# Optimization experiments

Hardware: AMD Instinct MI355X
Metric: run time of the kernel (lower is better)

The kernel has to match this reference:

```python
import jax, jax.numpy as jnp
import numpy as np

NPOINTS = 4096


def farthest_point_sample(inp, npoints):
    """Iterative farthest point sampling.
    inp: [B, N, 3] float. Returns (out [B, npoints, 3], idx [B, npoints] int32).
    Matches the CUDA kernel semantics: first selected index is 0, running
    min-squared-distance buffer initialized to a large value (temp=1e10),
    each step picks the point farthest from the selected set.
    """
    B, N, _ = inp.shape
    init_idx = jnp.zeros((B,), dtype=jnp.int32)
    dist0 = jnp.full((B, N), 1e10, dtype=inp.dtype)

    def step(carry, _):
        dist, last_idx = carry
        # gather last selected point per batch: [B, 1, 3]
        last_pt = jnp.take_along_axis(inp, last_idx[:, None, None].astype(jnp.int32), axis=1)
        d = jnp.sum((inp - last_pt) ** 2, axis=-1)  # [B, N]
        dist = jnp.minimum(dist, d)
        nxt = jnp.argmax(dist, axis=-1).astype(jnp.int32)  # [B]
        return (dist, nxt), nxt

    (_, _), rest = jax.lax.scan(step, (dist0, init_idx), None, length=npoints - 1)
    idx = jnp.concatenate([init_idx[None, :], rest], axis=0).T  # [B, npoints]
    out = jnp.take_along_axis(inp, idx[..., None], axis=1)  # [B, npoints, 3]
    return out, idx


def setup_inputs() -> dict:
    key = jax.random.key(0)
    inp = jax.random.normal(key, (32, 131072, 3), dtype=jnp.float32)
    return {"inp": inp}


def reference(inp):
    return farthest_point_sample(inp, NPOINTS)
```

## Files before the change

kernel.cpp:

```cpp
#include <hip/hip_runtime.h>
#include <stdint.h>

#define NBATCH  32
#define NPTS    131072
#define NPOINTS 4096
#define BPB     8
#define TPB     512
#define PPT     32
#define PPB     (NPTS / BPB)

typedef unsigned long long u64;
typedef unsigned int u32;


__global__ __attribute__((amdgpu_flat_work_group_size(TPB, TPB)))
           __attribute__((amdgpu_waves_per_eu(2, 2)))
void fps_kernel(const float* __restrict__ inp, float* __restrict__ out,
                u64* __restrict__ slots)
{
#pragma clang fp contract(off)
    const int bid  = blockIdx.x;
    const int b    = bid & 31;
    const int j    = bid >> 5;
    const int t    = threadIdx.x;
    const int lane = t & 63;
    const int wid  = t >> 6;

    const float* P  = inp + (size_t)b * NPTS * 3;
    float* outP     = out + (size_t)b * NPOINTS * 3;
    float* outIdx   = out + (size_t)NBATCH * NPOINTS * 3 + (size_t)b * NPOINTS;

    const int base = j * PPB;

    float px[PPT], py[PPT], pz[PPT], dist[PPT];
#pragma unroll
    for (int k = 0; k < PPT; ++k) {
        const int p = base + k * TPB + t;
        const float* pp = P + (size_t)p * 3;
        px[k] = pp[0]; py[k] = pp[1]; pz[k] = pp[2];
        asm volatile("" : "+v"(px[k]), "+v"(py[k]), "+v"(pz[k]));
        dist[k] = 1e10f;
    }

    float qx = P[0], qy = P[1], qz = P[2];

    if (j == 0 && t == 0) {
        outP[0] = qx; outP[1] = qy; outP[2] = qz;
        outIdx[0] = 0.0f;
    }

    u64* myslots = slots + (size_t)b * (2 * BPB * 2);

    __shared__ u64 skey[TPB / 64];
    __shared__ float sq[3];

    for (int it = 0; it < NPOINTS - 1; ++it) {
        float m = -1.0f; int ki = 0;
#pragma unroll
        for (int k = 0; k < PPT; ++k) {
            float dx = px[k] - qx;
            float dy = py[k] - qy;
            float dz = pz[k] - qz;
            float yy = dy * dy;
            asm("" : "+v"(yy));
            float d  = __builtin_fmaf(dz, dz,
                        __builtin_fmaf(dx, dx, yy));
            float nd = fminf(dist[k], d);
            dist[k] = nd;
            if (nd > m) { m = nd; ki = k; }
        }
        const int gi = base + ki * TPB + t;
        u64 key = ((u64)__float_as_uint(m) << 17) | (u64)(131071 - gi);

#pragma unroll
        for (int s = 1; s < 64; s <<= 1) {
            u64 o = __shfl_xor(key, s, 64);
            if (o > key) key = o;
        }
        if (lane == 0) skey[wid] = key;
        __syncthreads();

        if (wid == 0) {
            u64 k2 = (lane < TPB / 64) ? skey[lane] : 0ull;
#pragma unroll
            for (int s = 1; s < TPB / 64; s <<= 1) {
                u64 o = __shfl_xor(k2, s, 64);
                if (o > k2) k2 = o;
            }
            const int par = it & 1;
            const u64 tag = (u64)(it + 1) << 49;
            if (lane == 0) {
                __hip_atomic_store(&myslots[(par * BPB + j) * 2], tag | k2,
                                   __ATOMIC_RELEASE, __HIP_MEMORY_SCOPE_AGENT);
            }
            u64 v = 0;
            bool ok = (lane >= BPB);
            int guard = 0;
            while (true) {
                if (!ok) {
                    v = __hip_atomic_load(&myslots[(par * BPB + lane) * 2 + 0],
                                          __ATOMIC_ACQUIRE, __HIP_MEMORY_SCOPE_AGENT);
                    ok = (v >> 49) >= (u64)(it + 1);
                }
                if (__all((int)ok)) break;
                if (++guard > (1 << 20)) break;
            }
            u64 k3 = (lane < BPB) ? (v & ((1ull << 49) - 1)) : 0ull;
#pragma unroll
            for (int s = 1; s < BPB; s <<= 1) {
                u64 o = __shfl_xor(k3, s, 64);
                if (o > k3) k3 = o;
            }
            const int wgi = 131071 - (int)(k3 & 0x1FFFF);
            if (lane == 0) {
                const float* qp = P + (size_t)wgi * 3;
                float nqx = qp[0], nqy = qp[1], nqz = qp[2];
                sq[0] = nqx; sq[1] = nqy; sq[2] = nqz;
                if (j == 0) {
                    float* o3 = outP + (size_t)(it + 1) * 3;
                    o3[0] = nqx; o3[1] = nqy; o3[2] = nqz;
                    outIdx[it + 1] = (float)wgi;
                }
            }
        }
        __syncthreads();
        qx = sq[0]; qy = sq[1]; qz = sq[2];
    }
}

extern "C" void kernel_launch(void* const* d_in, const int* in_sizes, int n_in,
                              void* d_out, int out_size, void* d_ws, size_t ws_size,
                              hipStream_t stream)
{
    const float* inp = (const float*)d_in[0];
    float* outp      = (float*)d_out;
    u64* slots       = (u64*)d_ws;

    hipMemsetAsync(d_ws, 0, (size_t)NBATCH * 2 * BPB * 2 * sizeof(u64), stream);

    fps_kernel<<<NBATCH * BPB, TPB, 0, stream>>>(inp, outp, slots);
}
```

Measured before the change: 19.88 ms.

## Move point x,y coordinates from registers into LDS and pad sync slots

Per-thread x and y coordinates now live in shared memory as float2 and are read back each iteration, while z and the running distance stay in registers. The waves_per_eu hint is removed. Sync slots are spaced 8 u64 apart instead of 2, so each slot sits on its own 64-byte line. The aim is to cut VGPR pressure and reduce false sharing on the flags, at the cost of LDS reads in the hot loop and 128KB of LDS per block.

```diff
diff --git a/kernel.cpp b/kernel.cpp
--- a/kernel.cpp
+++ b/kernel.cpp
@@ -12,13 +12,16 @@
 typedef unsigned long long u64;
 typedef unsigned int u32;
 
+#define SLOT_STRIDE 8
+
 
 __global__ __attribute__((amdgpu_flat_work_group_size(TPB, TPB)))
-           __attribute__((amdgpu_waves_per_eu(2, 2)))
 void fps_kernel(const float* __restrict__ inp, float* __restrict__ out,
                 u64* __restrict__ slots)
 {
 #pragma clang fp contract(off)
+    extern __shared__ float2 XY[];
+
     const int bid  = blockIdx.x;
     const int b    = bid & 31;
     const int j    = bid >> 5;
@@ -32,13 +35,15 @@
 
     const int base = j * PPB;
 
-    float px[PPT], py[PPT], pz[PPT], dist[PPT];
+    float pz[PPT], dist[PPT];
 #pragma unroll
     for (int k = 0; k < PPT; ++k) {
-        const int p = base + k * TPB + t;
-        const float* pp = P + (size_t)p * 3;
-        px[k] = pp[0]; py[k] = pp[1]; pz[k] = pp[2];
-        asm volatile("" : "+v"(px[k]), "+v"(py[k]), "+v"(pz[k]));
+        const int l = k * TPB + t;
+        const float* pp = P + (size_t)(base + l) * 3;
+        float x = pp[0], y = pp[1], z = pp[2];
+        XY[l] = make_float2(x, y);
+        pz[k] = z;
+        asm volatile("" : "+v"(pz[k]));
         dist[k] = 1e10f;
     }
 
@@ -49,17 +54,20 @@
         outIdx[0] = 0.0f;
     }
 
-    u64* myslots = slots + (size_t)b * (2 * BPB * 2);
+    u64* myslots = slots + (size_t)b * (2 * BPB * SLOT_STRIDE);
 
     __shared__ u64 skey[TPB / 64];
     __shared__ float sq[3];
+
+    __syncthreads();
 
     for (int it = 0; it < NPOINTS - 1; ++it) {
         float m = -1.0f; int ki = 0;
 #pragma unroll
         for (int k = 0; k < PPT; ++k) {
-            float dx = px[k] - qx;
-            float dy = py[k] - qy;
+            float2 xy = XY[k * TPB + t];
+            float dx = xy.x - qx;
+            float dy = xy.y - qy;
             float dz = pz[k] - qz;
             float yy = dy * dy;
             asm("" : "+v"(yy));
@@ -90,7 +98,7 @@
             const int par = it & 1;
             const u64 tag = (u64)(it + 1) << 49;
             if (lane == 0) {
-                __hip_atomic_store(&myslots[(par * BPB + j) * 2], tag | k2,
+                __hip_atomic_store(&myslots[(par * BPB + j) * SLOT_STRIDE], tag | k2,
                                    __ATOMIC_RELEASE, __HIP_MEMORY_SCOPE_AGENT);
             }
             u64 v = 0;
@@ -98,7 +106,7 @@
             int guard = 0;
             while (true) {
                 if (!ok) {
-                    v = __hip_atomic_load(&myslots[(par * BPB + lane) * 2 + 0],
+                    v = __hip_atomic_load(&myslots[(par * BPB + lane) * SLOT_STRIDE],
                                           __ATOMIC_ACQUIRE, __HIP_MEMORY_SCOPE_AGENT);
                     ok = (v >> 49) >= (u64)(it + 1);
                 }
@@ -136,7 +144,8 @@
     float* outp      = (float*)d_out;
     u64* slots       = (u64*)d_ws;
 
-    hipMemsetAsync(d_ws, 0, (size_t)NBATCH * 2 * BPB * 2 * sizeof(u64), stream);
+    hipMemsetAsync(d_ws, 0,
+                   (size_t)NBATCH * 2 * BPB * SLOT_STRIDE * sizeof(u64), stream);
 
-    fps_kernel<<<NBATCH * BPB, TPB, 0, stream>>>(inp, outp, slots);
+    fps_kernel<<<NBATCH * BPB, TPB, (size_t)PPB * sizeof(float2), stream>>>(inp, outp, slots);
 }
```

Result: slower. 22.62 ms (+13.8%).

## Double blocks per batch and carry winner coordinates through reduction slots

Applied to the files above, without the earlier changes.

Splits each batch across 16 blocks instead of 8, with 16 points per thread, and raises waves per EU to 4. This spreads the per-iteration distance update over more CUs. Each thread now tracks the coordinates of its best point and passes them through the wave, block and cross-block reductions. The coordinates are published in padded global slots, so the dependent global gather of the winning point is no longer needed. The cost is more blocks taking part in the spin-wait barrier and extra slot stores and loads per iteration.

```diff
diff --git a/kernel.cpp b/kernel.cpp
--- a/kernel.cpp
+++ b/kernel.cpp
@@ -4,17 +4,19 @@
 #define NBATCH  32
 #define NPTS    131072
 #define NPOINTS 4096
-#define BPB     8
+#define BPB     16
 #define TPB     512
-#define PPT     32
+#define PPT     16
 #define PPB     (NPTS / BPB)
 
 typedef unsigned long long u64;
 typedef unsigned int u32;
 
+#define SLOT_STRIDE 8
+
 
 __global__ __attribute__((amdgpu_flat_work_group_size(TPB, TPB)))
-           __attribute__((amdgpu_waves_per_eu(2, 2)))
+           __attribute__((amdgpu_waves_per_eu(4, 4)))
 void fps_kernel(const float* __restrict__ inp, float* __restrict__ out,
                 u64* __restrict__ slots)
 {
@@ -38,24 +40,25 @@
         const int p = base + k * TPB + t;
         const float* pp = P + (size_t)p * 3;
         px[k] = pp[0]; py[k] = pp[1]; pz[k] = pp[2];
-        asm volatile("" : "+v"(px[k]), "+v"(py[k]), "+v"(pz[k]));
         dist[k] = 1e10f;
     }
 
     float qx = P[0], qy = P[1], qz = P[2];
-
     if (j == 0 && t == 0) {
         outP[0] = qx; outP[1] = qy; outP[2] = qz;
         outIdx[0] = 0.0f;
     }
 
-    u64* myslots = slots + (size_t)b * (2 * BPB * 2);
+    u64* myslots = slots + (size_t)b * (2 * BPB * SLOT_STRIDE);
 
     __shared__ u64 skey[TPB / 64];
+    __shared__ u64 sxy[TPB / 64];
+    __shared__ u64 sz[TPB / 64];
     __shared__ float sq[3];
 
     for (int it = 0; it < NPOINTS - 1; ++it) {
         float m = -1.0f; int ki = 0;
+        float mx = 0.f, my = 0.f, mz = 0.f;
 #pragma unroll
         for (int k = 0; k < PPT; ++k) {
             float dx = px[k] - qx;
@@ -67,59 +70,82 @@
                         __builtin_fmaf(dx, dx, yy));
             float nd = fminf(dist[k], d);
             dist[k] = nd;
-            if (nd > m) { m = nd; ki = k; }
+            bool c = nd > m;
+            m  = c ? nd : m;  ki = c ? k : ki;
+            mx = c ? px[k] : mx; my = c ? py[k] : my; mz = c ? pz[k] : mz;
         }
         const int gi = base + ki * TPB + t;
         u64 key = ((u64)__float_as_uint(m) << 17) | (u64)(131071 - gi);
 
+        u64 kmax = key;
 #pragma unroll
         for (int s = 1; s < 64; s <<= 1) {
-            u64 o = __shfl_xor(key, s, 64);
-            if (o > key) key = o;
+            u64 o = __shfl_xor(kmax, s, 64);
+            if (o > kmax) kmax = o;
         }
-        if (lane == 0) skey[wid] = key;
+        int wl = __ffsll(__ballot(key == kmax)) - 1;
+        float wx = __shfl(mx, wl, 64), wy = __shfl(my, wl, 64), wz = __shfl(mz, wl, 64);
+        if (lane == 0) {
+            skey[wid] = kmax;
+            sxy[wid]  = ((u64)__float_as_uint(wy) << 32) | __float_as_uint(wx);
+            sz[wid]   = __float_as_uint(wz);
+        }
         __syncthreads();
 
         if (wid == 0) {
             u64 k2 = (lane < TPB / 64) ? skey[lane] : 0ull;
+            u64 kk = k2;
 #pragma unroll
             for (int s = 1; s < TPB / 64; s <<= 1) {
-                u64 o = __shfl_xor(k2, s, 64);
-                if (o > k2) k2 = o;
+                u64 o = __shfl_xor(kk, s, 64);
+                if (o > kk) kk = o;
             }
+            int we = __ffsll(__ballot(k2 == kk && lane < TPB / 64)) - 1;
             const int par = it & 1;
             const u64 tag = (u64)(it + 1) << 49;
             if (lane == 0) {
-                __hip_atomic_store(&myslots[(par * BPB + j) * 2], tag | k2,
-                                   __ATOMIC_RELEASE, __HIP_MEMORY_SCOPE_AGENT);
+                u64* slot = &myslots[(size_t)(par * BPB + j) * SLOT_STRIDE];
+                __hip_atomic_store(&slot[1], sxy[we], __ATOMIC_RELAXED, __HIP_MEMORY_SCOPE_AGENT);
+                __hip_atomic_store(&slot[2], sz[we],  __ATOMIC_RELAXED, __HIP_MEMORY_SCOPE_AGENT);
+                __hip_atomic_store(&slot[0], tag | kk, __ATOMIC_RELEASE, __HIP_MEMORY_SCOPE_AGENT);
             }
-            u64 v = 0;
+            u64 tw = 0;
             bool ok = (lane >= BPB);
             int guard = 0;
             while (true) {
                 if (!ok) {
-                    v = __hip_atomic_load(&myslots[(par * BPB + lane) * 2 + 0],
-                                          __ATOMIC_ACQUIRE, __HIP_MEMORY_SCOPE_AGENT);
-                    ok = (v >> 49) >= (u64)(it + 1);
+                    tw = __hip_atomic_load(&myslots[(size_t)(par * BPB + lane) * SLOT_STRIDE],
+                                           __ATOMIC_ACQUIRE, __HIP_MEMORY_SCOPE_AGENT);
+                    ok = (tw >> 49) >= (u64)(it + 1);
                 }
                 if (__all((int)ok)) break;
                 if (++guard > (1 << 20)) break;
             }
-            u64 k3 = (lane < BPB) ? (v & ((1ull << 49) - 1)) : 0ull;
+            u64 pxy = 0, pzz = 0, k3 = 0;
+            if (lane < BPB) {
+                u64* slot = &myslots[(size_t)(par * BPB + lane) * SLOT_STRIDE];
+                pxy = __hip_atomic_load(&slot[1], __ATOMIC_RELAXED, __HIP_MEMORY_SCOPE_AGENT);
+                pzz = __hip_atomic_load(&slot[2], __ATOMIC_RELAXED, __HIP_MEMORY_SCOPE_AGENT);
+                k3  = tw & ((1ull << 49) - 1);
+            }
+            u64 k3m = k3;
 #pragma unroll
             for (int s = 1; s < BPB; s <<= 1) {
-                u64 o = __shfl_xor(k3, s, 64);
-                if (o > k3) k3 = o;
+                u64 o = __shfl_xor(k3m, s, 64);
+                if (o > k3m) k3m = o;
             }
-            const int wgi = 131071 - (int)(k3 & 0x1FFFF);
+            int w3 = __ffsll(__ballot(k3 == k3m && lane < BPB)) - 1;
+            u64 wxy = __shfl(pxy, w3, 64);
+            u64 wzz = __shfl(pzz, w3, 64);
             if (lane == 0) {
-                const float* qp = P + (size_t)wgi * 3;
-                float nqx = qp[0], nqy = qp[1], nqz = qp[2];
+                float nqx = __uint_as_float((u32)wxy);
+                float nqy = __uint_as_float((u32)(wxy >> 32));
+                float nqz = __uint_as_float((u32)wzz);
                 sq[0] = nqx; sq[1] = nqy; sq[2] = nqz;
                 if (j == 0) {
                     float* o3 = outP + (size_t)(it + 1) * 3;
                     o3[0] = nqx; o3[1] = nqy; o3[2] = nqz;
-                    outIdx[it + 1] = (float)wgi;
+                    outIdx[it + 1] = (float)(131071 - (int)(k3m & 0x1FFFF));
                 }
             }
         }
@@ -136,7 +162,8 @@
     float* outp      = (float*)d_out;
     u64* slots       = (u64*)d_ws;
 
-    hipMemsetAsync(d_ws, 0, (size_t)NBATCH * 2 * BPB * 2 * sizeof(u64), stream);
+    hipMemsetAsync(d_ws, 0,
+                   (size_t)NBATCH * 2 * BPB * SLOT_STRIDE * sizeof(u64), stream);
 
     fps_kernel<<<NBATCH * BPB, TPB, 0, stream>>>(inp, outp, slots);
 }
```

Result: slower. 54.79 ms (+175.6%).
